# Performance work log

Hardware: AMD Instinct MI355X
Metric: run time of the kernel (lower is better)

The kernel has to match this reference:

```python
import jax, jax.numpy as jnp
import numpy as np

EPS = 1e-8

def setup_inputs() -> dict:
    key = jax.random.key(0)
    ks = jax.random.split(key, 5)
    N, Cin, Cout, K, H, W = 16, 512, 512, 3, 64, 64
    return {
        "x": jax.random.normal(ks[0], (N, Cin, H, W), dtype=jnp.float32),
        "s": jax.random.normal(ks[1], (N, Cin), dtype=jnp.float32),
        "noise": jax.random.normal(ks[2], (N, Cout, H, W), dtype=jnp.float32),
        "w": jax.random.normal(ks[3], (Cout, Cin, K, K), dtype=jnp.float32),
        "b": jax.random.normal(ks[4], (Cout,), dtype=jnp.float32),
    }

def reference(x, s, noise, w, b):
    # Demodulation coefficient: d[n,o] = rsqrt(sum_{c,kh,kw} (w[o,c]*s[n,c])^2 + eps)
    # einsum: (s^2)[n,c] . (w^2 summed over kh,kw)[o,c] -> [n,o]
    w2 = jnp.sum(w * w, axis=(2, 3))                      # [Cout, Cin]
    d = jax.lax.rsqrt(jnp.einsum('nc,oc->no', s * s, w2) + EPS)  # [N, Cout]
    # Fold per-sample modulation into the input, demodulation into the output
    # (mathematically identical to grouped conv with per-sample modulated weights).
    x_mod = x * s[:, :, None, None]                       # [N, Cin, H, W]
    y = jax.lax.conv_general_dilated(
        x_mod, w,
        window_strides=(1, 1),
        padding='SAME',
        dimension_numbers=('NCHW', 'OIHW', 'NCHW'),
    )                                                     # [N, Cout, H, W]
    y = y * d[:, :, None, None] + b[None, :, None, None] + noise
    return jnp.where(y >= 0, y, 0.2 * y)  # LeakyReLU(0.2)
```

## Files before the change

### kernel.cpp

```cpp
#include <hip/hip_runtime.h>
#include <cstdint>
#include <cstddef>

typedef __attribute__((ext_vector_type(8))) short bf16x8;
typedef __attribute__((ext_vector_type(4))) float floatx4;

#define NBATCH 16
#define CIN    512
#define COUT   512
#define HH     64
#define WW     64
#define HP     66

#define XCOLS  72
#define XUS    (4 * XCOLS * 64)
#define AUS    (128 * 64)

static __device__ __forceinline__ unsigned short f2bf(float f) {
  union { float f; unsigned u; } cv; cv.f = f;
  unsigned u = cv.u;
  return (unsigned short)((u + 0x7FFFu + ((u >> 16) & 1u)) >> 16);
}

static __device__ __forceinline__ void async16(const unsigned short* g, unsigned short* l) {
  __builtin_amdgcn_global_load_lds(
      (const __attribute__((address_space(1))) void*)g,
      (__attribute__((address_space(3))) void*)l, 16, 0, 0);
}

__global__ void k_zero(unsigned short* __restrict__ xmp) {
  int slot = blockIdx.x;
  int n    = blockIdx.y;
  int h, w;
  if (slot < 66)       { h = 0;              w = slot;       }
  else if (slot < 132) { h = 65;             w = slot - 66;  }
  else if (slot < 196) { h = slot - 132 + 1; w = 0;          }
  else                 { h = slot - 196 + 1; w = 65;         }
  unsigned* p = (unsigned*)(xmp + (((size_t)n * HP + h) * HP + w) * CIN);
  p[threadIdx.x] = 0u;
}

__global__ void k_wprep(const float* __restrict__ w, unsigned short* __restrict__ wr,
                        float* __restrict__ w2t) {
  int o = blockIdx.x;
  int c = blockIdx.y * 256 + threadIdx.x;
  const float* wp = w + ((size_t)o * CIN + c) * 9;
  float v[9]; float sum = 0.f;
#pragma unroll
  for (int r = 0; r < 9; ++r) { v[r] = wp[r]; sum += v[r] * v[r]; }
  w2t[(size_t)c * COUT + o] = sum;
#pragma unroll
  for (int r = 0; r < 9; ++r)
    wr[((size_t)r * COUT + o) * CIN + c] = f2bf(v[r]);
}

__global__ void k_dcoef(const float* __restrict__ s, const float* __restrict__ w2t,
                        float* __restrict__ d) {
  __shared__ float s2[CIN];
  int n = blockIdx.y;
  int o = blockIdx.x * 256 + threadIdx.x;
  for (int c = threadIdx.x; c < CIN; c += 256) {
    float sv = s[n * CIN + c]; s2[c] = sv * sv;
  }
  __syncthreads();
  float sum = 0.f;
  for (int c = 0; c < CIN; ++c) sum += s2[c] * w2t[(size_t)c * COUT + o];
  d[n * COUT + o] = rsqrtf(sum + 1e-8f);
}

__global__ void k_xmod(const float* __restrict__ x, const float* __restrict__ s,
                       unsigned short* __restrict__ xmp) {
  __shared__ __align__(16) unsigned short tile[WW * 520];
  int tid  = threadIdx.x;
  int n    = blockIdx.x >> 6;
  int h    = blockIdx.x & 63;
  int wcol = tid & 63;
  int grp  = tid >> 6;
#pragma unroll
  for (int i = 0; i < 16; ++i) {
    int c0 = (i * 4 + grp) * 8;
    bf16x8 pk;
#pragma unroll
    for (int j = 0; j < 8; ++j) {
      int c = c0 + j;
      float v = x[(((size_t)n * CIN + c) * HH + h) * WW + wcol] * s[n * CIN + c];
      pk[j] = (short)f2bf(v);
    }
    *(bf16x8*)(tile + wcol * 520 + c0) = pk;
  }
  __syncthreads();
#pragma unroll
  for (int i = 0; i < 16; ++i) {
    int wv = i * 4 + grp;
    bf16x8 v = *(const bf16x8*)(tile + wv * 520 + wcol * 8);
    *(bf16x8*)(xmp + (((size_t)n * HP + (h + 1)) * HP + (wv + 1)) * CIN + wcol * 8) = v;
  }
}

__global__ __launch_bounds__(256, 2)
void k_conv(const unsigned short* __restrict__ xmp, const unsigned short* __restrict__ wr,
            const float* __restrict__ d, const float* __restrict__ bias,
            const float* __restrict__ noise, float* __restrict__ out) {
  __shared__ __align__(16) unsigned short smem[XUS + 2 * AUS];
  unsigned short* Xs  = smem;
  unsigned short* As0 = smem + XUS;
  unsigned short* As1 = smem + XUS + AUS;

  const int tid  = threadIdx.x;
  const int lane = tid & 63;
  const int l15  = lane & 15;
  const int quad = lane >> 4;
  const int wv   = tid >> 6;
  const int wrow = wv & 1;
  const int woc  = wv >> 1;

  const int bx  = blockIdx.x;
  const int n   = bx >> 5;
  const int h0  = (bx & 31) * 2;
  const int ocb = blockIdx.y * 128;

  floatx4 acc[4][4];
#pragma unroll
  for (int a = 0; a < 4; ++a)
#pragma unroll
    for (int b = 0; b < 4; ++b)
#pragma unroll
      for (int q = 0; q < 4; ++q) acc[a][b][q] = 0.f;

  auto stageX = [&](int cb) {
    const int c0 = cb * 64;
    const size_t grow = ((size_t)n * HP + (h0 + wv)) * HP;
#pragma unroll
    for (int t = 0; t < 9; ++t) {
      int ci   = t * 64 + lane;
      int col  = ci >> 3;
      int ch   = ci & 7;
      int colc = (col < 66) ? col : 65;
      const unsigned short* g = xmp + (grow + colc) * CIN + c0 + ((ch ^ (col & 7)) << 3);
      unsigned short* l = Xs + ((wv * 576 + t * 64) << 3);
      async16(g, l);
    }
  };
  auto stageW = [&](int r, int cb, unsigned short* buf) {
    const int c0 = cb * 64;
#pragma unroll
    for (int t = 0; t < 4; ++t) {
      int ci = wv * 256 + t * 64 + lane;
      int ol = ci >> 3;
      int ch = ci & 7;
      const unsigned short* g =
          wr + ((size_t)(r * COUT) + ocb + ol) * CIN + c0 + ((ch ^ (ol & 7)) << 3);
      unsigned short* l = buf + ((wv * 256 + t * 64) << 3);
      async16(g, l);
    }
  };

  unsigned short* Asel[2] = {As0, As1};

  stageX(0);
  stageW(0, 0, As0);

  for (int cb = 0; cb < 8; ++cb) {
#pragma unroll
    for (int r = 0; r < 9; ++r) {
      if (r < 8) stageW(r + 1, cb, Asel[(r + 1) & 1]);
      if (r < 8) asm volatile("s_waitcnt vmcnt(4)" ::: "memory");
      else       asm volatile("s_waitcnt vmcnt(0)" ::: "memory");
      __builtin_amdgcn_s_barrier();
      asm volatile("" ::: "memory");

      const unsigned short* Ab = Asel[r & 1];
      const int kh = r / 3, kw = r - (r / 3) * 3;
      const int xb = (wrow + kh) * XCOLS;
      __builtin_amdgcn_s_setprio(1);
#pragma unroll
      for (int ks = 0; ks < 2; ++ks) {
        bf16x8 af[4], bv[4];
#pragma unroll
        for (int mf = 0; mf < 4; ++mf) {
          int cpos = ((ks << 2) | quad) ^ (l15 & 7);
          af[mf] = *(const bf16x8*)(Ab + ((woc * 64 + mf * 16 + l15) << 6) + (cpos << 3));
        }
#pragma unroll
        for (int nf = 0; nf < 4; ++nf) {
          int slot = xb + nf * 16 + l15 + kw;
          int cpos = ((ks << 2) | quad) ^ ((l15 + kw) & 7);
          bv[nf] = *(const bf16x8*)(Xs + (slot << 6) + (cpos << 3));
        }
#pragma unroll
        for (int mf = 0; mf < 4; ++mf)
#pragma unroll
          for (int nf = 0; nf < 4; ++nf)
            acc[mf][nf] = __builtin_amdgcn_mfma_f32_16x16x32_bf16(af[mf], bv[nf], acc[mf][nf], 0, 0, 0);
      }
      __builtin_amdgcn_s_setprio(0);
      asm volatile("" ::: "memory");
      __builtin_amdgcn_s_barrier();
    }
    if (cb < 7) {
      stageX(cb + 1);
      stageW(0, cb + 1, As0);
    }
  }

  int h = h0 + wrow;
#pragma unroll
  for (int mf = 0; mf < 4; ++mf) {
#pragma unroll
    for (int i = 0; i < 4; ++i) {
      int o = ocb + woc * 64 + mf * 16 + quad * 4 + i;
      float dd = d[n * COUT + o];
      float bb = bias[o];
      size_t base = (((size_t)n * COUT + o) * HH + h) * WW;
#pragma unroll
      for (int nf = 0; nf < 4; ++nf) {
        int wc = nf * 16 + l15;
        float v = acc[mf][nf][i] * dd + bb + noise[base + wc];
        out[base + wc] = (v >= 0.f) ? v : 0.2f * v;
      }
    }
  }
}

extern "C" void kernel_launch(void* const* d_in, const int* in_sizes, int n_in,
                              void* d_out, int out_size, void* d_ws, size_t ws_size,
                              hipStream_t stream) {
  (void)in_sizes; (void)n_in; (void)out_size; (void)ws_size;
  const float* x     = (const float*)d_in[0];
  const float* s     = (const float*)d_in[1];
  const float* noise = (const float*)d_in[2];
  const float* w     = (const float*)d_in[3];
  const float* bias  = (const float*)d_in[4];
  float* out = (float*)d_out;

  char* ws = (char*)d_ws;
  const size_t XMP_BYTES = (size_t)NBATCH * HP * HP * CIN * 2;
  const size_t WR_BYTES  = (size_t)9 * COUT * CIN * 2;
  const size_t W2_BYTES  = (size_t)CIN * COUT * 4;
  unsigned short* xmp = (unsigned short*)ws;
  unsigned short* wrr = (unsigned short*)(ws + XMP_BYTES);
  float* w2t          = (float*)(ws + XMP_BYTES + WR_BYTES);
  float* dcoef        = (float*)(ws + XMP_BYTES + WR_BYTES + W2_BYTES);

  k_zero <<<dim3(260, NBATCH), 256, 0, stream>>>(xmp);
  k_wprep<<<dim3(COUT, 2),  256, 0, stream>>>(w, wrr, w2t);
  k_dcoef<<<dim3(2, NBATCH), 256, 0, stream>>>(s, w2t, dcoef);
  k_xmod <<<dim3(NBATCH * HH), 256, 0, stream>>>(x, s, xmp);
  k_conv <<<dim3(NBATCH * HH / 2, COUT / 128), 256, 0, stream>>>(xmp, wrr, dcoef, bias, noise, out);
}
```

Before: 599.6 us.

## Load weights directly into registers in MFMA fragment layout, double-buffer X tile

Weights are pre-packed into an MFMA fragment order so each wave loads its A operands straight from global memory into registers, prefetching the next tap while computing the current one. This removes the weight LDS staging and the two barriers per filter tap. LDS now double-buffers the input tile, with one barrier per channel block. The grid is flattened with a swizzled block index to group output-channel blocks for cache locality, and zero-padding runs in fewer blocks. The cost is more VGPR pressure, and weight loads come from L2 with no reuse across waves.

Measured after the change: 565.0 us. -5.8%, faster.

```diff
diff --git a/kernel.cpp b/kernel.cpp
--- a/kernel.cpp
+++ b/kernel.cpp
@@ -14,7 +14,6 @@
 
 #define XCOLS  72
 #define XUS    (4 * XCOLS * 64)
-#define AUS    (128 * 64)
 
 static __device__ __forceinline__ unsigned short f2bf(float f) {
   union { float f; unsigned u; } cv; cv.f = f;
@@ -30,17 +29,18 @@
 
 __global__ void k_zero(unsigned short* __restrict__ xmp) {
   int slot = blockIdx.x;
-  int n    = blockIdx.y;
   int h, w;
   if (slot < 66)       { h = 0;              w = slot;       }
   else if (slot < 132) { h = 65;             w = slot - 66;  }
   else if (slot < 196) { h = slot - 132 + 1; w = 0;          }
   else                 { h = slot - 196 + 1; w = 65;         }
-  unsigned* p = (unsigned*)(xmp + (((size_t)n * HP + h) * HP + w) * CIN);
-  p[threadIdx.x] = 0u;
-}
-
-__global__ void k_wprep(const float* __restrict__ w, unsigned short* __restrict__ wr,
+  for (int n = 0; n < NBATCH; ++n) {
+    unsigned* p = (unsigned*)(xmp + (((size_t)n * HP + h) * HP + w) * CIN);
+    p[threadIdx.x] = 0u;
+  }
+}
+
+__global__ void k_wprep(const float* __restrict__ w, unsigned short* __restrict__ wfrag,
                         float* __restrict__ w2t) {
   int o = blockIdx.x;
   int c = blockIdx.y * 256 + threadIdx.x;
@@ -49,9 +49,11 @@
 #pragma unroll
   for (int r = 0; r < 9; ++r) { v[r] = wp[r]; sum += v[r] * v[r]; }
   w2t[(size_t)c * COUT + o] = sum;
+  int ob = o >> 4, l15 = o & 15;
+  int cb = c >> 6, ks = (c >> 5) & 1, quad = (c >> 3) & 3, j = c & 7;
 #pragma unroll
   for (int r = 0; r < 9; ++r)
-    wr[((size_t)r * COUT + o) * CIN + c] = f2bf(v[r]);
+    wfrag[((((size_t)r * 8 + cb) * 32 + ob) * 2 + ks) * 512 + (quad * 16 + l15) * 8 + j] = f2bf(v[r]);
 }
 
 __global__ void k_dcoef(const float* __restrict__ s, const float* __restrict__ w2t,
@@ -98,13 +100,10 @@
 }
 
 __global__ __launch_bounds__(256, 2)
-void k_conv(const unsigned short* __restrict__ xmp, const unsigned short* __restrict__ wr,
+void k_conv(const unsigned short* __restrict__ xmp, const unsigned short* __restrict__ wfrag,
             const float* __restrict__ d, const float* __restrict__ bias,
             const float* __restrict__ noise, float* __restrict__ out) {
-  __shared__ __align__(16) unsigned short smem[XUS + 2 * AUS];
-  unsigned short* Xs  = smem;
-  unsigned short* As0 = smem + XUS;
-  unsigned short* As1 = smem + XUS + AUS;
+  __shared__ __align__(16) unsigned short smem[2 * XUS];
 
   const int tid  = threadIdx.x;
   const int lane = tid & 63;
@@ -114,10 +113,12 @@
   const int wrow = wv & 1;
   const int woc  = wv >> 1;
 
-  const int bx  = blockIdx.x;
-  const int n   = bx >> 5;
-  const int h0  = (bx & 31) * 2;
-  const int ocb = blockIdx.y * 128;
+  const int i    = blockIdx.x;
+  const int ybl  = (i & 7) >> 1;
+  const int lin  = ((i & 1) << 8) | (i >> 3);
+  const int n    = lin >> 5;
+  const int h0   = (lin & 31) * 2;
+  const int ob0  = ybl * 8 + woc * 4;
 
   floatx4 acc[4][4];
 #pragma unroll
@@ -127,7 +128,7 @@
 #pragma unroll
       for (int q = 0; q < 4; ++q) acc[a][b][q] = 0.f;
 
-  auto stageX = [&](int cb) {
+  auto stageX = [&](int cb, unsigned short* Xdst) {
     const int c0 = cb * 64;
     const size_t grow = ((size_t)n * HP + (h0 + wv)) * HP;
 #pragma unroll
@@ -137,50 +138,36 @@
       int ch   = ci & 7;
       int colc = (col < 66) ? col : 65;
       const unsigned short* g = xmp + (grow + colc) * CIN + c0 + ((ch ^ (col & 7)) << 3);
-      unsigned short* l = Xs + ((wv * 576 + t * 64) << 3);
-      async16(g, l);
+      async16(g, Xdst + ((wv * 576 + t * 64) << 3));
     }
   };
-  auto stageW = [&](int r, int cb, unsigned short* buf) {
-    const int c0 = cb * 64;
-#pragma unroll
-    for (int t = 0; t < 4; ++t) {
-      int ci = wv * 256 + t * 64 + lane;
-      int ol = ci >> 3;
-      int ch = ci & 7;
-      const unsigned short* g =
-          wr + ((size_t)(r * COUT) + ocb + ol) * CIN + c0 + ((ch ^ (ol & 7)) << 3);
-      unsigned short* l = buf + ((wv * 256 + t * 64) << 3);
-      async16(g, l);
-    }
+
+  auto loadW = [&](int r, int cb, bf16x8* dst) {
+#pragma unroll
+    for (int ks = 0; ks < 2; ++ks)
+#pragma unroll
+      for (int mf = 0; mf < 4; ++mf)
+        dst[ks * 4 + mf] = *(const bf16x8*)(
+            wfrag + ((((size_t)r * 8 + cb) * 32 + (ob0 + mf)) * 2 + ks) * 512 + lane * 8);
   };
 
-  unsigned short* Asel[2] = {As0, As1};
-
-  stageX(0);
-  stageW(0, 0, As0);
-
-  for (int cb = 0; cb < 8; ++cb) {
+  bf16x8 afA[8], afB[8];
+
+  auto convCB = [&](int cb, bf16x8* f0, bf16x8* f1) {
+    unsigned short* Xs = smem + (cb & 1) * XUS;
+    if (cb < 7) stageX(cb + 1, smem + ((cb + 1) & 1) * XUS);
 #pragma unroll
     for (int r = 0; r < 9; ++r) {
-      if (r < 8) stageW(r + 1, cb, Asel[(r + 1) & 1]);
-      if (r < 8) asm volatile("s_waitcnt vmcnt(4)" ::: "memory");
-      else       asm volatile("s_waitcnt vmcnt(0)" ::: "memory");
-      __builtin_amdgcn_s_barrier();
-      asm volatile("" ::: "memory");
-
-      const unsigned short* Ab = Asel[r & 1];
+      bf16x8* cur = (r & 1) ? f1 : f0;
+      bf16x8* nxt = (r & 1) ? f0 : f1;
+      if (r < 8)      loadW(r + 1, cb, nxt);
+      else if (cb < 7) loadW(0, cb + 1, nxt);
       const int kh = r / 3, kw = r - (r / 3) * 3;
       const int xb = (wrow + kh) * XCOLS;
       __builtin_amdgcn_s_setprio(1);
 #pragma unroll
       for (int ks = 0; ks < 2; ++ks) {
-        bf16x8 af[4], bv[4];
-#pragma unroll
-        for (int mf = 0; mf < 4; ++mf) {
-          int cpos = ((ks << 2) | quad) ^ (l15 & 7);
-          af[mf] = *(const bf16x8*)(Ab + ((woc * 64 + mf * 16 + l15) << 6) + (cpos << 3));
-        }
+        bf16x8 bv[4];
 #pragma unroll
         for (int nf = 0; nf < 4; ++nf) {
           int slot = xb + nf * 16 + l15 + kw;
@@ -191,31 +178,41 @@
         for (int mf = 0; mf < 4; ++mf)
 #pragma unroll
           for (int nf = 0; nf < 4; ++nf)
-            acc[mf][nf] = __builtin_amdgcn_mfma_f32_16x16x32_bf16(af[mf], bv[nf], acc[mf][nf], 0, 0, 0);
+            acc[mf][nf] = __builtin_amdgcn_mfma_f32_16x16x32_bf16(cur[ks * 4 + mf], bv[nf], acc[mf][nf], 0, 0, 0);
       }
       __builtin_amdgcn_s_setprio(0);
-      asm volatile("" ::: "memory");
-      __builtin_amdgcn_s_barrier();
-    }
-    if (cb < 7) {
-      stageX(cb + 1);
-      stageW(0, cb + 1, As0);
-    }
+    }
+    asm volatile("s_waitcnt vmcnt(0)" ::: "memory");
+    __builtin_amdgcn_s_barrier();
+    asm volatile("" ::: "memory");
+  };
+
+  stageX(0, smem);
+  loadW(0, 0, afA);
+  asm volatile("s_waitcnt vmcnt(0)" ::: "memory");
+  __builtin_amdgcn_s_barrier();
+  asm volatile("" ::: "memory");
+
+#pragma unroll 1
+  for (int c2 = 0; c2 < 4; ++c2) {
+    convCB(2 * c2,     afA, afB);
+    convCB(2 * c2 + 1, afB, afA);
   }
 
   int h = h0 + wrow;
+  int ocb = ybl * 128;
 #pragma unroll
   for (int mf = 0; mf < 4; ++mf) {
 #pragma unroll
-    for (int i = 0; i < 4; ++i) {
-      int o = ocb + woc * 64 + mf * 16 + quad * 4 + i;
+    for (int ii = 0; ii < 4; ++ii) {
+      int o = ocb + woc * 64 + mf * 16 + quad * 4 + ii;
       float dd = d[n * COUT + o];
       float bb = bias[o];
       size_t base = (((size_t)n * COUT + o) * HH + h) * WW;
 #pragma unroll
       for (int nf = 0; nf < 4; ++nf) {
         int wc = nf * 16 + l15;
-        float v = acc[mf][nf][i] * dd + bb + noise[base + wc];
+        float v = acc[mf][nf][ii] * dd + bb + noise[base + wc];
         out[base + wc] = (v >= 0.f) ? v : 0.2f * v;
       }
     }
@@ -235,16 +232,16 @@
 
   char* ws = (char*)d_ws;
   const size_t XMP_BYTES = (size_t)NBATCH * HP * HP * CIN * 2;
-  const size_t WR_BYTES  = (size_t)9 * COUT * CIN * 2;
+  const size_t WF_BYTES  = (size_t)9 * COUT * CIN * 2;
   const size_t W2_BYTES  = (size_t)CIN * COUT * 4;
-  unsigned short* xmp = (unsigned short*)ws;
-  unsigned short* wrr = (unsigned short*)(ws + XMP_BYTES);
-  float* w2t          = (float*)(ws + XMP_BYTES + WR_BYTES);
-  float* dcoef        = (float*)(ws + XMP_BYTES + WR_BYTES + W2_BYTES);
-
-  k_zero <<<dim3(260, NBATCH), 256, 0, stream>>>(xmp);
-  k_wprep<<<dim3(COUT, 2),  256, 0, stream>>>(w, wrr, w2t);
+  unsigned short* xmp   = (unsigned short*)ws;
+  unsigned short* wfrag = (unsigned short*)(ws + XMP_BYTES);
+  float* w2t            = (float*)(ws + XMP_BYTES + WF_BYTES);
+  float* dcoef          = (float*)(ws + XMP_BYTES + WF_BYTES + W2_BYTES);
+
+  k_zero <<<dim3(260),       256, 0, stream>>>(xmp);
+  k_wprep<<<dim3(COUT, 2),   256, 0, stream>>>(w, wfrag, w2t);
   k_dcoef<<<dim3(2, NBATCH), 256, 0, stream>>>(s, w2t, dcoef);
   k_xmod <<<dim3(NBATCH * HH), 256, 0, stream>>>(x, s, xmp);
-  k_conv <<<dim3(NBATCH * HH / 2, COUT / 128), 256, 0, stream>>>(xmp, wrr, dcoef, bias, noise, out);
-}
+  k_conv <<<dim3(NBATCH * HH / 2 * (COUT / 128)), 256, 0, stream>>>(xmp, wfrag, dcoef, bias, noise, out);
+}
```
